# Performance work log

Hardware: AMD Instinct MI355X
Metric: run time of the kernel (lower is better)

## Reference

```python
import jax, jax.numpy as jnp
import numpy as np

EPS = 1e-5

def _bn(h, g, b, m, v):
    # h: (B, Ch, L); BatchNorm1d in eval mode over channel axis 1
    inv = jax.lax.rsqrt(v + EPS)
    return (h - m[None, :, None]) * (inv * g)[None, :, None] + b[None, :, None]

def setup_inputs() -> dict:
    key = jax.random.key(0)
    ks = jax.random.split(key, 12)
    B, C, N = 32, 256, 4096
    N8, C8 = N // 8, C // 8
    x = jax.random.normal(ks[0], (B, C, N), dtype=jnp.float32)
    Wq = jax.random.normal(ks[1], (N8, N), dtype=jnp.float32) * (1.0 / np.sqrt(N))
    Wk = jax.random.normal(ks[2], (N8, N), dtype=jnp.float32) * (1.0 / np.sqrt(N))
    bn1_g = jnp.ones((N8,), jnp.float32); bn1_b = jnp.zeros((N8,), jnp.float32)
    bn1_m = jax.random.normal(ks[3], (N8,), jnp.float32) * 0.1
    bn1_v = jax.random.uniform(ks[4], (N8,), jnp.float32, 0.5, 1.5)
    bn2_g = jnp.ones((N8,), jnp.float32); bn2_b = jnp.zeros((N8,), jnp.float32)
    bn2_m = jax.random.normal(ks[5], (N8,), jnp.float32) * 0.1
    bn2_v = jax.random.uniform(ks[6], (N8,), jnp.float32, 0.5, 1.5)
    W1 = jax.random.normal(ks[7], (C8, C), dtype=jnp.float32) * (1.0 / np.sqrt(C))
    W2 = jax.random.normal(ks[8], (C, C8), dtype=jnp.float32) * (1.0 / np.sqrt(C8))
    alpha = jax.random.normal(ks[9], (1,), dtype=jnp.float32)
    return {"x": x, "Wq": Wq, "bn1_g": bn1_g, "bn1_b": bn1_b, "bn1_m": bn1_m, "bn1_v": bn1_v,
            "Wk": Wk, "bn2_g": bn2_g, "bn2_b": bn2_b, "bn2_m": bn2_m, "bn2_v": bn2_v,
            "W1": W1, "W2": W2, "alpha": alpha}

def reference(x, Wq, bn1_g, bn1_b, bn1_m, bn1_v, Wk, bn2_g, bn2_b, bn2_m, bn2_v, W1, W2, alpha):
    # x: (B, C, N); x_hat: (B, N, C) -- conv1d with kernel 1 == matmul over N axis
    x_hat = jnp.transpose(x, (0, 2, 1))
    q = jax.nn.relu(_bn(jnp.einsum('qn,bnc->bqc', Wq, x_hat), bn1_g, bn1_b, bn1_m, bn1_v))  # (B, N8, C)
    k = jax.nn.relu(_bn(jnp.einsum('qn,bnc->bqc', Wk, x_hat), bn2_g, bn2_b, bn2_m, bn2_v))  # (B, N8, C)
    sim = jnp.einsum('bkc,bkd->bcd', k, q)  # (B, C, C)
    aff = jax.nn.softmax(jnp.max(sim, axis=-1, keepdims=True) - sim, axis=-1)
    # squeeze-excite gating over channels
    pooled = jnp.max(x, axis=-1)  # (B, C) AdaptiveMaxPool1d(1)
    s = jax.nn.sigmoid(jax.nn.relu(pooled @ W1.T) @ W2.T)  # (B, C)
    gated = x * s[:, :, None]
    out = alpha[0] * jnp.einsum('bcd,bdn->bcn', aff, gated) + x
    return out
```

## Files before the change

kernel.cpp:

```cpp
#include <hip/hip_runtime.h>
#include <math.h>

#define B_   32
#define C_   256
#define N_   4096
#define N8_  512
#define C8_  32
#define EPS_ 1e-5f

typedef __attribute__((ext_vector_type(8))) short short8;
typedef __attribute__((ext_vector_type(4))) float f32x4;

__device__ __forceinline__ ushort f2bf(float v) {
  unsigned u = __float_as_uint(v);
  unsigned r = (u + 0x7fffu + ((u >> 16) & 1u)) >> 16;
  return (ushort)r;
}
__device__ __forceinline__ float bf2f(ushort h) {
  return __uint_as_float(((unsigned)h) << 16);
}

__global__ __launch_bounds__(256) void k_cvt(const float* __restrict__ src,
                                             ushort* __restrict__ hi,
                                             ushort* __restrict__ lo, int n4) {
  int i = blockIdx.x * 256 + threadIdx.x;
  int stride = gridDim.x * 256;
  for (; i < n4; i += stride) {
    float4 v = ((const float4*)src)[i];
    ushort4 h, l;
    h.x = f2bf(v.x); l.x = f2bf(v.x - bf2f(h.x));
    h.y = f2bf(v.y); l.y = f2bf(v.y - bf2f(h.y));
    h.z = f2bf(v.z); l.z = f2bf(v.z - bf2f(h.z));
    h.w = f2bf(v.w); l.w = f2bf(v.w - bf2f(h.w));
    ((ushort4*)hi)[i] = h;
    ((ushort4*)lo)[i] = l;
  }
}

__global__ __launch_bounds__(256) void k_cvt_x(const float* __restrict__ x,
    ushort* __restrict__ xh, ushort* __restrict__ xl,
    ushort* __restrict__ xTh, float* __restrict__ partial) {
  int b = blockIdx.z, cb = blockIdx.y, nb = blockIdx.x;
  int t = threadIdx.x;
  int cl  = t >> 2;
  int nl0 = (t & 3) * 16;
  const float* xp = x + ((size_t)b * C_ + cb * 64 + cl) * N_ + nb * 64 + nl0;
  float v[16];
  *(float4*)&v[0]  = *(const float4*)(xp + 0);
  *(float4*)&v[4]  = *(const float4*)(xp + 4);
  *(float4*)&v[8]  = *(const float4*)(xp + 8);
  *(float4*)&v[12] = *(const float4*)(xp + 12);
  ushort h[16], l[16];
  float mx = -3.402823466e+38f;
  #pragma unroll
  for (int j = 0; j < 16; ++j) {
    h[j] = f2bf(v[j]);
    l[j] = f2bf(v[j] - bf2f(h[j]));
    mx = fmaxf(mx, v[j]);
  }
  size_t fbase = ((size_t)b * C_ + cb * 64 + cl) * N_ + nb * 64 + nl0;
  *(short8*)(xh + fbase)     = *(short8*)&h[0];
  *(short8*)(xh + fbase + 8) = *(short8*)&h[8];
  *(short8*)(xl + fbase)     = *(short8*)&l[0];
  *(short8*)(xl + fbase + 8) = *(short8*)&l[8];
  mx = fmaxf(mx, __shfl_xor(mx, 1, 64));
  mx = fmaxf(mx, __shfl_xor(mx, 2, 64));
  if ((t & 3) == 0)
    partial[((size_t)b * C_ + cb * 64 + cl) * 64 + nb] = mx;
  __shared__ ushort lds[64 * 66];
  #pragma unroll
  for (int j = 0; j < 16; ++j) lds[cl * 66 + nl0 + j] = h[j];
  __syncthreads();
  int nr = t >> 2;
  int c0 = (t & 3) * 16;
  ushort o[16];
  #pragma unroll
  for (int j = 0; j < 16; ++j) o[j] = lds[(c0 + j) * 66 + nr];
  size_t tbase = ((size_t)b * N_ + nb * 64 + nr) * C_ + cb * 64 + c0;
  *(short8*)(xTh + tbase)     = *(short8*)&o[0];
  *(short8*)(xTh + tbase + 8) = *(short8*)&o[8];
}

__global__ __launch_bounds__(256) void k_semlp(const float* __restrict__ partial,
                                               const float* __restrict__ W1,
                                               const float* __restrict__ W2,
                                               float* __restrict__ s) {
  int b = blockIdx.x, t = threadIdx.x;
  __shared__ float p[C_];
  __shared__ float h[C8_];
  float m = -3.402823466e+38f;
  const float* pp = partial + ((size_t)b * C_ + t) * 64;
  #pragma unroll
  for (int j = 0; j < 64; ++j) m = fmaxf(m, pp[j]);
  p[t] = m;
  __syncthreads();
  if (t < C8_) {
    float a = 0.f;
    for (int c = 0; c < C_; ++c) a = fmaf(p[c], W1[t * C_ + c], a);
    h[t] = fmaxf(a, 0.f);
  }
  __syncthreads();
  float a = 0.f;
  #pragma unroll
  for (int j = 0; j < C8_; ++j) a = fmaf(h[j], W2[t * C8_ + j], a);
  s[b * C_ + t] = 1.f / (1.f + __expf(-a));
}

#define GLD16(SRC, DSTP) __builtin_amdgcn_global_load_lds( \
    (const __attribute__((address_space(1))) void*)(SRC), \
    (__attribute__((address_space(3))) void*)(DSTP), 16, 0, 0)

__global__ __launch_bounds__(512, 2) void k_qk8(
    const ushort* __restrict__ wh, const ushort* __restrict__ wl,
    const ushort* __restrict__ xh, const ushort* __restrict__ xl,
    float* __restrict__ part) {
  __shared__ ushort lds[2][2][256 * 64];
  const int ks = blockIdx.x;
  const int mt = blockIdx.y;
  const int b  = blockIdx.z;
  const int t = threadIdx.x;
  const int lane = t & 63, wave = t >> 6;
  const int wm = wave >> 2, wn = wave & 3;
  const int fr = lane & 15, quad = lane >> 4;
  const int R0 = mt * 256;
  const int tr = t >> 3, tc = (t & 7) << 3;
  int aro[4], bro[4];
#pragma unroll
  for (int j = 0; j < 4; ++j) {
    int rl = j * 64 + tr;
    int cu = tc ^ ((rl & 7) << 3);
    aro[j] = (R0 + rl) * N_ + cu;
    bro[j] = (b * C_ + rl) * N_ + cu;
  }
  const int dl = t * 8;

  f32x4 acc[8][4];
#pragma unroll
  for (int m = 0; m < 8; ++m)
#pragma unroll
    for (int n = 0; n < 4; ++n) acc[m][n] = (f32x4){0.f, 0.f, 0.f, 0.f};

  short8 af[4][2];
  short8 bf[2][2][2];

#define STG_A(AP, K0, P, J0) do { \
    GLD16((AP) + (aro[J0] + (K0)), &lds[P][0][(J0) * 4096 + dl]); \
    GLD16((AP) + (aro[(J0) + 1] + (K0)), &lds[P][0][((J0) + 1) * 4096 + dl]); \
  } while (0)
#define STG_B(BP, K0, P, J0) do { \
    GLD16((BP) + (bro[J0] + (K0)), &lds[P][1][(J0) * 4096 + dl]); \
    GLD16((BP) + (bro[(J0) + 1] + (K0)), &lds[P][1][((J0) + 1) * 4096 + dl]); \
  } while (0)
#define VMC(N) asm volatile("s_waitcnt vmcnt(" #N ")" ::: "memory")
#define BARF() do { __builtin_amdgcn_s_barrier(); \
                    __builtin_amdgcn_sched_barrier(0); } while (0)
#define RDA(P, MH) do { \
    _Pragma("unroll") \
    for (int m = 0; m < 4; ++m) { \
      int r = wm * 128 + ((MH) * 4 + m) * 16 + fr; \
      int o = (r << 6); \
      int sw = (r & 7) << 3; \
      af[m][0] = *(const short8*)&lds[P][0][o + ((quad << 3) ^ sw)]; \
      af[m][1] = *(const short8*)&lds[P][0][o + (((quad << 3) + 32) ^ sw)]; \
    } } while (0)
#define RDB(P, NH) do { \
    _Pragma("unroll") \
    for (int n = 0; n < 2; ++n) { \
      int c = wn * 64 + ((NH) * 2 + n) * 16 + fr; \
      int o = (c << 6); \
      int sw = (c & 7) << 3; \
      bf[NH][n][0] = *(const short8*)&lds[P][1][o + ((quad << 3) ^ sw)]; \
      bf[NH][n][1] = *(const short8*)&lds[P][1][o + (((quad << 3) + 32) ^ sw)]; \
    } } while (0)
#define MMQ(MH, NH) do { \
    __builtin_amdgcn_s_setprio(1); \
    _Pragma("unroll") \
    for (int m = 0; m < 4; ++m) \
      _Pragma("unroll") \
      for (int n = 0; n < 2; ++n) { \
        acc[(MH)*4+m][(NH)*2+n] = __builtin_amdgcn_mfma_f32_16x16x32_bf16( \
            af[m][0], bf[NH][n][0], acc[(MH)*4+m][(NH)*2+n], 0, 0, 0); \
        acc[(MH)*4+m][(NH)*2+n] = __builtin_amdgcn_mfma_f32_16x16x32_bf16( \
            af[m][1], bf[NH][n][1], acc[(MH)*4+m][(NH)*2+n], 0, 0, 0); \
      } \
    __builtin_amdgcn_s_setprio(0); } while (0)

  const int gbase = ks * 96;
  {
    int g = gbase, sg = g >> 6, k0 = (g & 63) << 6;
    const ushort* Ap = (sg == 1) ? wl : wh;
    const ushort* Bp = (sg == 2) ? xl : xh;
    STG_A(Ap, k0, 0, 0); STG_A(Ap, k0, 0, 2);
    STG_B(Bp, k0, 0, 0); STG_B(Bp, k0, 0, 2);
    int g1 = gbase + 1, s1 = g1 >> 6, k1 = (g1 & 63) << 6;
    const ushort* Ap1 = (s1 == 1) ? wl : wh;
    STG_A(Ap1, k1, 1, 0);
  }

#pragma unroll 1
  for (int i = 0; i < 48; ++i) {
    int gO = gbase + 2 * i + 1, sO = gO >> 6, kO = (gO & 63) << 6;
    const ushort* AO = (sO == 1) ? wl : wh;
    const ushort* BO = (sO == 2) ? xl : xh;
    int gE = gbase + 2 * i + 2, sE = gE >> 6, kE = (gE & 63) << 6;
    const ushort* AE = (sE == 1) ? wl : wh;
    const ushort* BE = (sE == 2) ? xl : xh;
    int gP = gbase + 2 * i + 3, sP = gP >> 6, kP = (gP & 63) << 6;
    const ushort* APn = (sP == 1) ? wl : wh;
    const bool nl = (i < 47);
    STG_A(AO, kO, 1, 2);
    VMC(4); BARF();
    RDA(0, 0); RDB(0, 0); MMQ(0, 0);
    STG_B(BO, kO, 1, 0);
    RDB(0, 1); MMQ(0, 1);
    STG_B(BO, kO, 1, 2);
    RDA(0, 1); MMQ(1, 0);
    BARF();
    if (nl) STG_A(AE, kE, 0, 0);
    MMQ(1, 1);
    if (nl) { STG_A(AE, kE, 0, 2); VMC(4); } else { VMC(0); }
    BARF();
    RDA(1, 0); RDB(1, 0); MMQ(0, 0);
    if (nl) STG_B(BE, kE, 0, 0);
    RDB(1, 1); MMQ(0, 1);
    if (nl) STG_B(BE, kE, 0, 2);
    RDA(1, 1); MMQ(1, 0);
    BARF();
    if (nl) STG_A(APn, kP, 1, 0);
    MMQ(1, 1);
  }

  float* dst = part + ((size_t)(ks * 32 + b) * 1024) * 256;
#pragma unroll
  for (int m = 0; m < 8; ++m) {
    int row0 = R0 + wm * 128 + m * 16 + quad * 4;
#pragma unroll
    for (int r = 0; r < 4; ++r) {
#pragma unroll
      for (int n = 0; n < 4; ++n) {
        int col = wn * 64 + n * 16 + fr;
        dst[(size_t)(row0 + r) * 256 + col] = acc[m][n][r];
      }
    }
  }
#undef STG_A
#undef STG_B
#undef VMC
#undef BARF
#undef RDA
#undef RDB
#undef MMQ
}

__global__ __launch_bounds__(256) void k_qkred(
    const float* __restrict__ part,
    const float* __restrict__ g1, const float* __restrict__ b1,
    const float* __restrict__ m1, const float* __restrict__ v1,
    const float* __restrict__ g2, const float* __restrict__ b2,
    const float* __restrict__ m2, const float* __restrict__ v2,
    float* __restrict__ q, float* __restrict__ k) {
  int i = blockIdx.x * 256 + threadIdx.x;
  int b = i >> 16;
  int rem = i & 65535;
  int row = rem >> 6;
  int c4 = (rem & 63) << 2;
  const float4* p = (const float4*)part;
  float4 u = p[i];
  float4 w = p[i + 2097152];
  bool isq = row < 512;
  int m = isq ? row : row - 512;
  float sc = (isq ? g1 : g2)[m] * rsqrtf((isq ? v1 : v2)[m] + EPS_);
  float bi = (isq ? b1 : b2)[m] - (isq ? m1 : m2)[m] * sc;
  float4 o;
  o.x = fmaxf(fmaf(u.x + w.x, sc, bi), 0.f);
  o.y = fmaxf(fmaf(u.y + w.y, sc, bi), 0.f);
  o.z = fmaxf(fmaf(u.z + w.z, sc, bi), 0.f);
  o.w = fmaxf(fmaf(u.w + w.w, sc, bi), 0.f);
  float* d = (isq ? q : k) + ((size_t)b * N8_ + m) * C_ + c4;
  *(float4*)d = o;
}

__global__ __launch_bounds__(256) void k_simsoft(const float* __restrict__ q,
    const float* __restrict__ k, const float* __restrict__ s,
    const float* __restrict__ alpha, ushort* __restrict__ aff2) {
  int b = blockIdx.y, ct = blockIdx.x;
  int t = threadIdx.x;
  __shared__ float kT[N8_][16];
  const float* kb = k + (size_t)b * N8_ * C_;
  int c0 = ct * 16;
  for (int chunk = 0; chunk < N8_ / 16; ++chunk) {
    int row = chunk * 16 + (t >> 4);
    kT[row][t & 15] = kb[(size_t)row * C_ + c0 + (t & 15)];
  }
  __syncthreads();
  float acc[16];
  #pragma unroll
  for (int i = 0; i < 16; ++i) acc[i] = 0.f;
  const float* qb = q + (size_t)b * N8_ * C_;
  for (int kk = 0; kk < N8_; ++kk) {
    float qv = qb[(size_t)kk * C_ + t];
    float4 k0 = *(const float4*)&kT[kk][0];
    float4 k1 = *(const float4*)&kT[kk][4];
    float4 k2 = *(const float4*)&kT[kk][8];
    float4 k3 = *(const float4*)&kT[kk][12];
    acc[0]  = fmaf(k0.x, qv, acc[0]);  acc[1]  = fmaf(k0.y, qv, acc[1]);
    acc[2]  = fmaf(k0.z, qv, acc[2]);  acc[3]  = fmaf(k0.w, qv, acc[3]);
    acc[4]  = fmaf(k1.x, qv, acc[4]);  acc[5]  = fmaf(k1.y, qv, acc[5]);
    acc[6]  = fmaf(k1.z, qv, acc[6]);  acc[7]  = fmaf(k1.w, qv, acc[7]);
    acc[8]  = fmaf(k2.x, qv, acc[8]);  acc[9]  = fmaf(k2.y, qv, acc[9]);
    acc[10] = fmaf(k2.z, qv, acc[10]); acc[11] = fmaf(k2.w, qv, acc[11]);
    acc[12] = fmaf(k3.x, qv, acc[12]); acc[13] = fmaf(k3.y, qv, acc[13]);
    acc[14] = fmaf(k3.z, qv, acc[14]); acc[15] = fmaf(k3.w, qv, acc[15]);
  }
  int lane = t & 63, wid = t >> 6;
  __shared__ float wmin[16][4];
  __shared__ float wsum[16][4];
  #pragma unroll
  for (int i = 0; i < 16; ++i) {
    float v = acc[i];
    for (int off = 32; off > 0; off >>= 1) v = fminf(v, __shfl_xor(v, off, 64));
    if (lane == 0) wmin[i][wid] = v;
  }
  __syncthreads();
  float w[16];
  #pragma unroll
  for (int i = 0; i < 16; ++i) {
    float m = fminf(fminf(wmin[i][0], wmin[i][1]), fminf(wmin[i][2], wmin[i][3]));
    w[i] = __expf(m - acc[i]);
  }
  #pragma unroll
  for (int i = 0; i < 16; ++i) {
    float v = w[i];
    for (int off = 32; off > 0; off >>= 1) v += __shfl_xor(v, off, 64);
    if (lane == 0) wsum[i][wid] = v;
  }
  __syncthreads();
  float fac = alpha[0] * s[b * C_ + t];
  ushort* ab = aff2 + (size_t)b * C_ * C_;
  #pragma unroll
  for (int i = 0; i < 16; ++i) {
    float Z = wsum[i][0] + wsum[i][1] + wsum[i][2] + wsum[i][3];
    ab[(size_t)(c0 + i) * C_ + t] = f2bf(fac * w[i] / Z);
  }
}

__global__ __launch_bounds__(256) void k_out_mfma(
    const ushort* __restrict__ aff, const ushort* __restrict__ xTh,
    const float* __restrict__ x, float* __restrict__ out) {
  int b  = blockIdx.z;
  int cb = blockIdx.y;
  int nb = blockIdx.x;
  __shared__ ushort Ah[128 * 32];
  __shared__ ushort Bh[128 * 32];
  int t = threadIdx.x, wave = t >> 6, lane = t & 63;
  int wr = (wave >> 1) * 64, wc = (wave & 1) * 64;
  int srow = wave * 16 + (lane >> 2);
  int skof = (lane & 3) * 8;
  size_t aoff = ((size_t)b * C_ + cb * 128 + srow) * C_ + skof;
  size_t boff = ((size_t)b * N_ + nb * 128 + srow) * C_ + skof;
  int lb0 = (wave * 16) * 32;

  f32x4 acc[4][4];
  #pragma unroll
  for (int mi = 0; mi < 4; ++mi)
    #pragma unroll
    for (int ni = 0; ni < 4; ++ni)
      acc[mi][ni] = (f32x4){0.f, 0.f, 0.f, 0.f};

  int fr = lane & 15, quad = lane >> 4;
  for (int k0 = 0; k0 < C_; k0 += 32) {
    #pragma unroll
    for (int seg = 0; seg < 2; ++seg) {
      size_t ga = aoff + (size_t)seg * 64 * C_ + k0;
      size_t gb = boff + (size_t)seg * 64 * C_ + k0;
      int lb = lb0 + seg * 64 * 32;
      __builtin_amdgcn_global_load_lds(
          (const __attribute__((address_space(1))) void*)(aff + ga),
          (__attribute__((address_space(3))) void*)(&Ah[lb]), 16, 0, 0);
      __builtin_amdgcn_global_load_lds(
          (const __attribute__((address_space(1))) void*)(xTh + gb),
          (__attribute__((address_space(3))) void*)(&Bh[lb]), 16, 0, 0);
    }
    __syncthreads();
    short8 af[4], bf[4];
    #pragma unroll
    for (int i = 0; i < 4; ++i) {
      af[i] = *(const short8*)&Ah[(wr + i * 16 + fr) * 32 + quad * 8];
      bf[i] = *(const short8*)&Bh[(wc + i * 16 + fr) * 32 + quad * 8];
    }
    #pragma unroll
    for (int mi = 0; mi < 4; ++mi)
      #pragma unroll
      for (int ni = 0; ni < 4; ++ni)
        acc[mi][ni] = __builtin_amdgcn_mfma_f32_16x16x32_bf16(
            af[mi], bf[ni], acc[mi][ni], 0, 0, 0);
    __syncthreads();
  }

  const float* xb = x + (size_t)b * C_ * N_;
  float* ob = out + (size_t)b * C_ * N_;
  int c0 = cb * 128 + wr + quad * 4;
  int n0 = nb * 128 + wc + fr;
  #pragma unroll
  for (int mi = 0; mi < 4; ++mi) {
    #pragma unroll
    for (int r = 0; r < 4; ++r) {
      int c = c0 + mi * 16 + r;
      #pragma unroll
      for (int ni = 0; ni < 4; ++ni) {
        int n = n0 + ni * 16;
        ob[(size_t)c * N_ + n] = acc[mi][ni][r] + xb[(size_t)c * N_ + n];
      }
    }
  }
}

extern "C" void kernel_launch(void* const* d_in, const int* in_sizes, int n_in,
                              void* d_out, int out_size, void* d_ws, size_t ws_size,
                              hipStream_t stream) {
  const float* x     = (const float*)d_in[0];
  const float* Wq    = (const float*)d_in[1];
  const float* g1    = (const float*)d_in[2];
  const float* b1    = (const float*)d_in[3];
  const float* m1    = (const float*)d_in[4];
  const float* v1    = (const float*)d_in[5];
  const float* Wk    = (const float*)d_in[6];
  const float* g2    = (const float*)d_in[7];
  const float* b2    = (const float*)d_in[8];
  const float* m2    = (const float*)d_in[9];
  const float* v2    = (const float*)d_in[10];
  const float* W1    = (const float*)d_in[11];
  const float* W2    = (const float*)d_in[12];
  const float* alpha = (const float*)d_in[13];
  float* out = (float*)d_out;

  float* ws      = (float*)d_ws;
  float* q       = ws;
  float* kbuf    = q + (size_t)B_ * N8_ * C_;
  float* partial = kbuf + (size_t)B_ * N8_ * C_;
  float* s       = partial + (size_t)B_ * C_ * 64;
  ushort* aff    = (ushort*)(s + B_ * C_);
  ushort* xh     = aff + (size_t)B_ * C_ * C_;
  ushort* xl     = xh + (size_t)B_ * C_ * N_;
  ushort* xTh    = xl + (size_t)B_ * C_ * N_;
  ushort* wh     = xTh + (size_t)B_ * C_ * N_;
  ushort* wl     = wh + (size_t)2 * N8_ * N_;

  float* gpart = (float*)d_out;

  k_cvt_x<<<dim3(64, 4, B_), 256, 0, stream>>>(x, xh, xl, xTh, partial);
  k_cvt<<<dim3(1024), 256, 0, stream>>>(Wq, wh, wl, N8_ * N_ / 4);
  k_cvt<<<dim3(1024), 256, 0, stream>>>(Wk, wh + (size_t)N8_ * N_,
                                        wl + (size_t)N8_ * N_, N8_ * N_ / 4);
  k_semlp<<<dim3(B_), 256, 0, stream>>>(partial, W1, W2, s);
  k_qk8<<<dim3(2, 4, B_), 512, 0, stream>>>(wh, wl, xh, xl, gpart);
  k_qkred<<<dim3(8192), 256, 0, stream>>>(gpart, g1, b1, m1, v1,
                                          g2, b2, m2, v2, q, kbuf);
  k_simsoft<<<dim3(16, B_), 256, 0, stream>>>(q, kbuf, s, alpha, aff);
  k_out_mfma<<<dim3(32, 2, B_), 256, 0, stream>>>(aff, xTh, x, out);
}
```

Before: 663.0 us.

## Drop split-K in QK GEMM, fuse BN+ReLU epilogue, XCD-aware block mapping

The QK projection GEMM no longer splits K in two with partial sums written to a scratch buffer. Each block now covers the full K range on a 256x128 output tile, halved along N, and applies the batchnorm scale/bias and ReLU directly in its epilogue. This removes the separate reduction kernel and the round-trip of partials through global memory. Blocks are remapped so each XCD handles four batches, which should improve L2 reuse of the x tiles, at the cost of a longer serial K loop per block and less A-tile reuse per block.

```diff
diff --git a/kernel.cpp b/kernel.cpp
--- a/kernel.cpp
+++ b/kernel.cpp
@@ -113,43 +113,53 @@
 __global__ __launch_bounds__(512, 2) void k_qk8(
     const ushort* __restrict__ wh, const ushort* __restrict__ wl,
     const ushort* __restrict__ xh, const ushort* __restrict__ xl,
-    float* __restrict__ part) {
-  __shared__ ushort lds[2][2][256 * 64];
-  const int ks = blockIdx.x;
-  const int mt = blockIdx.y;
-  const int b  = blockIdx.z;
+    const float* __restrict__ g1, const float* __restrict__ b1,
+    const float* __restrict__ m1, const float* __restrict__ v1,
+    const float* __restrict__ g2, const float* __restrict__ b2,
+    const float* __restrict__ m2, const float* __restrict__ v2,
+    float* __restrict__ q, float* __restrict__ k) {
+  __shared__ ushort lds[2][24576];
+  const int bid = blockIdx.x;
+  const int xcd = bid & 7, slot = bid >> 3;
+  const int b  = xcd * 4 + (slot & 3);
+  const int rr_ = slot >> 2;
+  const int mt = rr_ >> 1, nt = rr_ & 1;
   const int t = threadIdx.x;
   const int lane = t & 63, wave = t >> 6;
   const int wm = wave >> 2, wn = wave & 3;
   const int fr = lane & 15, quad = lane >> 4;
-  const int R0 = mt * 256;
   const int tr = t >> 3, tc = (t & 7) << 3;
-  int aro[4], bro[4];
+  int aro[4], bro[2];
 #pragma unroll
   for (int j = 0; j < 4; ++j) {
     int rl = j * 64 + tr;
     int cu = tc ^ ((rl & 7) << 3);
-    aro[j] = (R0 + rl) * N_ + cu;
-    bro[j] = (b * C_ + rl) * N_ + cu;
+    aro[j] = (mt * 256 + rl) * N_ + cu;
+  }
+#pragma unroll
+  for (int j = 0; j < 2; ++j) {
+    int rl = j * 64 + tr;
+    int cu = tc ^ ((rl & 7) << 3);
+    bro[j] = (b * C_ + nt * 128 + rl) * N_ + cu;
   }
   const int dl = t * 8;
 
-  f32x4 acc[8][4];
+  f32x4 acc[8][2];
 #pragma unroll
   for (int m = 0; m < 8; ++m)
 #pragma unroll
-    for (int n = 0; n < 4; ++n) acc[m][n] = (f32x4){0.f, 0.f, 0.f, 0.f};
+    for (int n = 0; n < 2; ++n) acc[m][n] = (f32x4){0.f, 0.f, 0.f, 0.f};
 
   short8 af[4][2];
-  short8 bf[2][2][2];
-
-#define STG_A(AP, K0, P, J0) do { \
-    GLD16((AP) + (aro[J0] + (K0)), &lds[P][0][(J0) * 4096 + dl]); \
-    GLD16((AP) + (aro[(J0) + 1] + (K0)), &lds[P][0][((J0) + 1) * 4096 + dl]); \
+  short8 bf[2][2];
+
+#define STG_A2(AP, K0, P, J0) do { \
+    GLD16((AP) + (aro[J0] + (K0)), &lds[P][(J0) * 4096 + dl]); \
+    GLD16((AP) + (aro[(J0) + 1] + (K0)), &lds[P][((J0) + 1) * 4096 + dl]); \
   } while (0)
-#define STG_B(BP, K0, P, J0) do { \
-    GLD16((BP) + (bro[J0] + (K0)), &lds[P][1][(J0) * 4096 + dl]); \
-    GLD16((BP) + (bro[(J0) + 1] + (K0)), &lds[P][1][((J0) + 1) * 4096 + dl]); \
+#define STG_B2(BP, K0, P) do { \
+    GLD16((BP) + (bro[0] + (K0)), &lds[P][16384 + dl]); \
+    GLD16((BP) + (bro[1] + (K0)), &lds[P][16384 + 4096 + dl]); \
   } while (0)
 #define VMC(N) asm volatile("s_waitcnt vmcnt(" #N ")" ::: "memory")
 #define BARF() do { __builtin_amdgcn_s_barrier(); \
@@ -160,124 +170,88 @@
       int r = wm * 128 + ((MH) * 4 + m) * 16 + fr; \
       int o = (r << 6); \
       int sw = (r & 7) << 3; \
-      af[m][0] = *(const short8*)&lds[P][0][o + ((quad << 3) ^ sw)]; \
-      af[m][1] = *(const short8*)&lds[P][0][o + (((quad << 3) + 32) ^ sw)]; \
+      af[m][0] = *(const short8*)&lds[P][o + ((quad << 3) ^ sw)]; \
+      af[m][1] = *(const short8*)&lds[P][o + (((quad << 3) + 32) ^ sw)]; \
     } } while (0)
-#define RDB(P, NH) do { \
+#define RDB(P) do { \
     _Pragma("unroll") \
     for (int n = 0; n < 2; ++n) { \
-      int c = wn * 64 + ((NH) * 2 + n) * 16 + fr; \
-      int o = (c << 6); \
+      int c = wn * 32 + n * 16 + fr; \
+      int o = 16384 + (c << 6); \
       int sw = (c & 7) << 3; \
-      bf[NH][n][0] = *(const short8*)&lds[P][1][o + ((quad << 3) ^ sw)]; \
-      bf[NH][n][1] = *(const short8*)&lds[P][1][o + (((quad << 3) + 32) ^ sw)]; \
+      bf[n][0] = *(const short8*)&lds[P][o + ((quad << 3) ^ sw)]; \
+      bf[n][1] = *(const short8*)&lds[P][o + (((quad << 3) + 32) ^ sw)]; \
     } } while (0)
 #define MMQ(MH, NH) do { \
     __builtin_amdgcn_s_setprio(1); \
     _Pragma("unroll") \
-    for (int m = 0; m < 4; ++m) \
-      _Pragma("unroll") \
-      for (int n = 0; n < 2; ++n) { \
-        acc[(MH)*4+m][(NH)*2+n] = __builtin_amdgcn_mfma_f32_16x16x32_bf16( \
-            af[m][0], bf[NH][n][0], acc[(MH)*4+m][(NH)*2+n], 0, 0, 0); \
-        acc[(MH)*4+m][(NH)*2+n] = __builtin_amdgcn_mfma_f32_16x16x32_bf16( \
-            af[m][1], bf[NH][n][1], acc[(MH)*4+m][(NH)*2+n], 0, 0, 0); \
-      } \
+    for (int m = 0; m < 4; ++m) { \
+      acc[(MH)*4+m][NH] = __builtin_amdgcn_mfma_f32_16x16x32_bf16( \
+          af[m][0], bf[NH][0], acc[(MH)*4+m][NH], 0, 0, 0); \
+      acc[(MH)*4+m][NH] = __builtin_amdgcn_mfma_f32_16x16x32_bf16( \
+          af[m][1], bf[NH][1], acc[(MH)*4+m][NH], 0, 0, 0); \
+    } \
     __builtin_amdgcn_s_setprio(0); } while (0)
 
-  const int gbase = ks * 96;
-  {
-    int g = gbase, sg = g >> 6, k0 = (g & 63) << 6;
-    const ushort* Ap = (sg == 1) ? wl : wh;
-    const ushort* Bp = (sg == 2) ? xl : xh;
-    STG_A(Ap, k0, 0, 0); STG_A(Ap, k0, 0, 2);
-    STG_B(Bp, k0, 0, 0); STG_B(Bp, k0, 0, 2);
-    int g1 = gbase + 1, s1 = g1 >> 6, k1 = (g1 & 63) << 6;
-    const ushort* Ap1 = (s1 == 1) ? wl : wh;
-    STG_A(Ap1, k1, 1, 0);
-  }
+  STG_A2(wh, 0, 0, 0); STG_A2(wh, 0, 0, 2); STG_B2(xh, 0, 0);
+  STG_A2(wh, 64, 1, 0);
 
 #pragma unroll 1
-  for (int i = 0; i < 48; ++i) {
-    int gO = gbase + 2 * i + 1, sO = gO >> 6, kO = (gO & 63) << 6;
+  for (int i = 0; i < 96; ++i) {
+    int gO = 2 * i + 1, sO = gO >> 6, kO = (gO & 63) << 6;
     const ushort* AO = (sO == 1) ? wl : wh;
     const ushort* BO = (sO == 2) ? xl : xh;
-    int gE = gbase + 2 * i + 2, sE = gE >> 6, kE = (gE & 63) << 6;
+    int gE = 2 * i + 2, sE = gE >> 6, kE = (gE & 63) << 6;
     const ushort* AE = (sE == 1) ? wl : wh;
     const ushort* BE = (sE == 2) ? xl : xh;
-    int gP = gbase + 2 * i + 3, sP = gP >> 6, kP = (gP & 63) << 6;
+    int gP = 2 * i + 3, sP = gP >> 6, kP = (gP & 63) << 6;
     const ushort* APn = (sP == 1) ? wl : wh;
-    const bool nl = (i < 47);
-    STG_A(AO, kO, 1, 2);
+    const bool nl = (i < 95);
+    STG_A2(AO, kO, 1, 2);
     VMC(4); BARF();
-    RDA(0, 0); RDB(0, 0); MMQ(0, 0);
-    STG_B(BO, kO, 1, 0);
-    RDB(0, 1); MMQ(0, 1);
-    STG_B(BO, kO, 1, 2);
+    RDA(0, 0); RDB(0); MMQ(0, 0);
+    STG_B2(BO, kO, 1);
+    MMQ(0, 1);
     RDA(0, 1); MMQ(1, 0);
     BARF();
-    if (nl) STG_A(AE, kE, 0, 0);
+    if (nl) STG_A2(AE, kE, 0, 0);
     MMQ(1, 1);
-    if (nl) { STG_A(AE, kE, 0, 2); VMC(4); } else { VMC(0); }
+    if (nl) { STG_A2(AE, kE, 0, 2); VMC(4); } else { VMC(0); }
     BARF();
-    RDA(1, 0); RDB(1, 0); MMQ(0, 0);
-    if (nl) STG_B(BE, kE, 0, 0);
-    RDB(1, 1); MMQ(0, 1);
-    if (nl) STG_B(BE, kE, 0, 2);
+    RDA(1, 0); RDB(1); MMQ(0, 0);
+    if (nl) STG_B2(BE, kE, 0);
+    MMQ(0, 1);
     RDA(1, 1); MMQ(1, 0);
     BARF();
-    if (nl) STG_A(APn, kP, 1, 0);
+    if (nl) STG_A2(APn, kP, 1, 0);
     MMQ(1, 1);
   }
 
-  float* dst = part + ((size_t)(ks * 32 + b) * 1024) * 256;
 #pragma unroll
   for (int m = 0; m < 8; ++m) {
-    int row0 = R0 + wm * 128 + m * 16 + quad * 4;
+    int row0 = mt * 256 + wm * 128 + m * 16 + quad * 4;
 #pragma unroll
     for (int r = 0; r < 4; ++r) {
-#pragma unroll
-      for (int n = 0; n < 4; ++n) {
-        int col = wn * 64 + n * 16 + fr;
-        dst[(size_t)(row0 + r) * 256 + col] = acc[m][n][r];
+      int row = row0 + r;
+      bool isq = row < N8_;
+      int mi = isq ? row : row - N8_;
+      float sc = (isq ? g1 : g2)[mi] * rsqrtf((isq ? v1 : v2)[mi] + EPS_);
+      float bi = (isq ? b1 : b2)[mi] - (isq ? m1 : m2)[mi] * sc;
+      float* dp = (isq ? q : k) + ((size_t)b * N8_ + mi) * C_;
+#pragma unroll
+      for (int n = 0; n < 2; ++n) {
+        int col = nt * 128 + wn * 32 + n * 16 + fr;
+        dp[col] = fmaxf(fmaf(acc[m][n][r], sc, bi), 0.f);
       }
     }
   }
-#undef STG_A
-#undef STG_B
+#undef STG_A2
+#undef STG_B2
 #undef VMC
 #undef BARF
 #undef RDA
 #undef RDB
 #undef MMQ
-}
-
-__global__ __launch_bounds__(256) void k_qkred(
-    const float* __restrict__ part,
-    const float* __restrict__ g1, const float* __restrict__ b1,
-    const float* __restrict__ m1, const float* __restrict__ v1,
-    const float* __restrict__ g2, const float* __restrict__ b2,
-    const float* __restrict__ m2, const float* __restrict__ v2,
-    float* __restrict__ q, float* __restrict__ k) {
-  int i = blockIdx.x * 256 + threadIdx.x;
-  int b = i >> 16;
-  int rem = i & 65535;
-  int row = rem >> 6;
-  int c4 = (rem & 63) << 2;
-  const float4* p = (const float4*)part;
-  float4 u = p[i];
-  float4 w = p[i + 2097152];
-  bool isq = row < 512;
-  int m = isq ? row : row - 512;
-  float sc = (isq ? g1 : g2)[m] * rsqrtf((isq ? v1 : v2)[m] + EPS_);
-  float bi = (isq ? b1 : b2)[m] - (isq ? m1 : m2)[m] * sc;
-  float4 o;
-  o.x = fmaxf(fmaf(u.x + w.x, sc, bi), 0.f);
-  o.y = fmaxf(fmaf(u.y + w.y, sc, bi), 0.f);
-  o.z = fmaxf(fmaf(u.z + w.z, sc, bi), 0.f);
-  o.w = fmaxf(fmaf(u.w + w.w, sc, bi), 0.f);
-  float* d = (isq ? q : k) + ((size_t)b * N8_ + m) * C_ + c4;
-  *(float4*)d = o;
 }
 
 __global__ __launch_bounds__(256) void k_simsoft(const float* __restrict__ q,
@@ -446,16 +420,14 @@
   ushort* wh     = xTh + (size_t)B_ * C_ * N_;
   ushort* wl     = wh + (size_t)2 * N8_ * N_;
 
-  float* gpart = (float*)d_out;
-
   k_cvt_x<<<dim3(64, 4, B_), 256, 0, stream>>>(x, xh, xl, xTh, partial);
   k_cvt<<<dim3(1024), 256, 0, stream>>>(Wq, wh, wl, N8_ * N_ / 4);
   k_cvt<<<dim3(1024), 256, 0, stream>>>(Wk, wh + (size_t)N8_ * N_,
                                         wl + (size_t)N8_ * N_, N8_ * N_ / 4);
   k_semlp<<<dim3(B_), 256, 0, stream>>>(partial, W1, W2, s);
-  k_qk8<<<dim3(2, 4, B_), 512, 0, stream>>>(wh, wl, xh, xl, gpart);
-  k_qkred<<<dim3(8192), 256, 0, stream>>>(gpart, g1, b1, m1, v1,
-                                          g2, b2, m2, v2, q, kbuf);
+  k_qk8<<<dim3(256), 512, 0, stream>>>(wh, wl, xh, xl,
+                                       g1, b1, m1, v1,
+                                       g2, b2, m2, v2, q, kbuf);
   k_simsoft<<<dim3(16, B_), 256, 0, stream>>>(q, kbuf, s, alpha, aff);
   k_out_mfma<<<dim3(32, 2, B_), 256, 0, stream>>>(aff, xTh, x, out);
 }
```

New measurement: 670.1 us. About the same (+1.1%).
